# Kernel tuning notes

Measured on AMD Instinct MI355X. Metric: run time of the kernel, lower is better.

Reference implementation:

```python
import jax, jax.numpy as jnp
import numpy as np

N, E, D, H = 50000, 800000, 128, 4
C = D // H  # per-head out channels
NEG_SLOPE = 0.2
BN_EPS = 1e-5


def _glorot(key, shape, fan):
    return jax.random.normal(key, shape, jnp.float32) / np.sqrt(fan)


def setup_inputs() -> dict:
    key = jax.random.key(0)
    ks = jax.random.split(key, 8)
    inp = {
        'x': jax.random.normal(ks[0], (N, D), jnp.float32),
        'edge_index': jax.random.randint(ks[1], (2, E), 0, N, dtype=jnp.int32),
        'Wl1': _glorot(ks[2], (D, D), D), 'Wr1': _glorot(ks[3], (D, D), D),
        'att1': _glorot(ks[4], (H, C), C), 'b1': jnp.zeros((D,), jnp.float32),
        'gamma1': jnp.ones((D,), jnp.float32), 'beta1': jnp.zeros((D,), jnp.float32),
        'Wl2': _glorot(ks[5], (D, D), D), 'Wr2': _glorot(ks[6], (D, D), D),
        'att2': _glorot(ks[7], (H, C), C), 'b2': jnp.zeros((D,), jnp.float32),
        'gamma2': jnp.ones((D,), jnp.float32), 'beta2': jnp.zeros((D,), jnp.float32),
    }
    return inp


def gatv2_conv(x, src, dst, Wl, Wr, att, bias):
    # PyG GATv2Conv, concat=True, add_self_loops handled by caller.
    n = x.shape[0]
    xl = (x @ Wl).reshape(n, H, C)  # source-side transform
    xr = (x @ Wr).reshape(n, H, C)  # target-side transform
    e = xl[src] + xr[dst]                      # [E', H, C]
    e = jnp.where(e > 0, e, NEG_SLOPE * e)     # LeakyReLU
    logits = jnp.einsum('ehc,hc->eh', e, att)  # [E', H]
    # segment softmax over destination node
    m = jax.ops.segment_max(logits, dst, num_segments=n)  # [N, H]
    ex = jnp.exp(logits - m[dst])
    den = jax.ops.segment_sum(ex, dst, num_segments=n)
    alpha = ex / den[dst]                      # [E', H]
    out = jax.ops.segment_sum(alpha[:, :, None] * xl[src], dst, num_segments=n)
    return out.reshape(n, H * C) + bias


def batchnorm(x, gamma, beta):
    mu = x.mean(0)
    var = x.var(0)
    return gamma * (x - mu) * jax.lax.rsqrt(var + BN_EPS) + beta


def reference(x, edge_index, Wl1, Wr1, att1, b1, gamma1, beta1,
              Wl2, Wr2, att2, b2, gamma2, beta2):
    n = x.shape[0]
    loop = jnp.arange(n, dtype=edge_index.dtype)
    src = jnp.concatenate([edge_index[0], loop])  # add self-loops (PyG default)
    dst = jnp.concatenate([edge_index[1], loop])
    identity = x
    out = gatv2_conv(x, src, dst, Wl1, Wr1, att1, b1)
    out = jax.nn.relu(batchnorm(out, gamma1, beta1))
    out = gatv2_conv(out, src, dst, Wl2, Wr2, att2, b2)
    out = batchnorm(out, gamma2, beta2) + identity
    return jax.nn.relu(out)
```

## Files before the change

kernel.cpp:

```cpp
#include <hip/hip_runtime.h>
#include <cstdint>
#include <cstddef>

#define D 128
#define BN_EPS 1e-5f
#define NEG_INF -3.0e38f
#define BN_BLOCKS 512

typedef __attribute__((ext_vector_type(8))) short bf16x8;
typedef __attribute__((ext_vector_type(4))) float f32x4;

static __device__ __forceinline__ unsigned short f2bf(float f) {
    uint32_t u = __float_as_uint(f);
    uint32_t r = (u + 0x7fffu + ((u >> 16) & 1u)) >> 16;
    return (unsigned short)r;
}

static __device__ __forceinline__ float hsum16(float x) {
    x += __int_as_float(__builtin_amdgcn_update_dpp(0, __float_as_int(x), 0xB1, 0xF, 0xF, true));
    x += __int_as_float(__builtin_amdgcn_update_dpp(0, __float_as_int(x), 0x4E, 0xF, 0xF, true));
    x += __int_as_float(__builtin_amdgcn_update_dpp(0, __float_as_int(x), 0x124, 0xF, 0xF, true));
    x += __int_as_float(__builtin_amdgcn_update_dpp(0, __float_as_int(x), 0x128, 0xF, 0xF, true));
    return x;
}

__global__ void zero_kernel(int* cnt, int n, int* esrc_tail) {
    int i = blockIdx.x * 256 + threadIdx.x;
    if (i < n) cnt[i] = 0;
    if (i < 16) esrc_tail[i] = 0;
}

__global__ void hist_kernel(const int* __restrict__ dst, int* __restrict__ cnt, int E) {
    int e = blockIdx.x * 256 + threadIdx.x;
    if (e < E) atomicAdd(&cnt[dst[e]], 1);
}

__global__ void scan_block(const int* __restrict__ cnt, int* __restrict__ row_start,
                           int* __restrict__ bsum, int n) {
    __shared__ int tmp[256];
    int tid = threadIdx.x;
    int i = blockIdx.x * 256 + tid;
    int v = (i < n) ? cnt[i] : 0;
    tmp[tid] = v; __syncthreads();
    for (int off = 1; off < 256; off <<= 1) {
        int t = (tid >= off) ? tmp[tid - off] : 0;
        __syncthreads();
        tmp[tid] += t; __syncthreads();
    }
    if (i < n) row_start[i + 1] = tmp[tid];
    if (tid == 255) bsum[blockIdx.x] = tmp[255];
}

__global__ void scan_bsum(int* bsum, int nb) {
    __shared__ int tmp[256];
    int tid = threadIdx.x;
    int v = (tid < nb) ? bsum[tid] : 0;
    tmp[tid] = v; __syncthreads();
    for (int off = 1; off < 256; off <<= 1) {
        int t = (tid >= off) ? tmp[tid - off] : 0;
        __syncthreads();
        tmp[tid] += t; __syncthreads();
    }
    if (tid < nb) bsum[tid] = tmp[tid];
}

__global__ void scan_fix(int* __restrict__ row_start, const int* __restrict__ bsum,
                         int* __restrict__ cursor, int n) {
    int i = blockIdx.x * 256 + threadIdx.x;
    if (i < n) {
        int add = (blockIdx.x > 0) ? bsum[blockIdx.x - 1] : 0;
        int val = row_start[i + 1] + add;
        row_start[i + 1] = val;
        if (i + 1 < n) cursor[i + 1] = val;
    }
    if (i == 0) { row_start[0] = 0; cursor[0] = 0; }
}

__global__ void scatter_kernel(const int* __restrict__ src, const int* __restrict__ dst,
                               int* __restrict__ cursor, int* __restrict__ esrc, int E) {
    int e = blockIdx.x * 256 + threadIdx.x;
    if (e < E) {
        int p = atomicAdd(&cursor[dst[e]], 1);
        esrc[p] = src[e];
    }
}

__global__ void repack_w(const float* __restrict__ Wl, const float* __restrict__ Wr,
                         unsigned short* __restrict__ Bp) {
    int idx = blockIdx.x * 256 + threadIdx.x;
    int i    = idx & 7;
    int lane = (idx >> 3) & 63;
    int kt   = (idx >> 9) & 3;
    int jt   = idx >> 11;
    int k   = kt * 32 + (lane >> 4) * 8 + i;
    int col = jt * 16 + (lane & 15);
    float v = (col < 128) ? Wl[k * 128 + col] : Wr[k * 128 + (col - 128)];
    Bp[idx] = f2bf(v);
}

template<bool BN>
__global__ __launch_bounds__(256, 2) void gemm_mfma(
    const float* __restrict__ X, const unsigned short* __restrict__ Bp,
    const float* __restrict__ scale, const float* __restrict__ shift,
    unsigned short* __restrict__ xl, float* __restrict__ xr, int n)
{
    __shared__ unsigned short smem[32768];
    {
        const float4* s = (const float4*)Bp;
        float4* d = (float4*)smem;
        #pragma unroll
        for (int it = 0; it < 16; ++it)
            d[it * 256 + threadIdx.x] = s[it * 256 + threadIdx.x];
    }
    __syncthreads();

    int wid = threadIdx.x >> 6, lane = threadIdx.x & 63;
    int nw = (n + 31) >> 5;
    int wrow = blockIdx.x * 4 + wid;
    if (wrow >= nw) return;
    int r0 = wrow * 32;
    int m = lane & 15, hi = lane >> 4;

    f32x4 accA[16], accB[16];
    #pragma unroll
    for (int jt = 0; jt < 16; ++jt) {
        accA[jt] = (f32x4){0.f, 0.f, 0.f, 0.f};
        accB[jt] = (f32x4){0.f, 0.f, 0.f, 0.f};
    }

    int rA = r0 + m;      if (rA > n - 1) rA = n - 1;
    int rB = r0 + 16 + m; if (rB > n - 1) rB = n - 1;
    const float* xrowA = X + (size_t)rA * D;
    const float* xrowB = X + (size_t)rB * D;

    #pragma unroll
    for (int kt = 0; kt < 4; ++kt) {
        int kb = kt * 32 + hi * 8;
        float sca[8], shf[8];
        if (BN) {
            float4 s0 = *(const float4*)(scale + kb);
            float4 s1 = *(const float4*)(scale + kb + 4);
            float4 h0 = *(const float4*)(shift + kb);
            float4 h1 = *(const float4*)(shift + kb + 4);
            sca[0]=s0.x; sca[1]=s0.y; sca[2]=s0.z; sca[3]=s0.w;
            sca[4]=s1.x; sca[5]=s1.y; sca[6]=s1.z; sca[7]=s1.w;
            shf[0]=h0.x; shf[1]=h0.y; shf[2]=h0.z; shf[3]=h0.w;
            shf[4]=h1.x; shf[5]=h1.y; shf[6]=h1.z; shf[7]=h1.w;
        }
        float4 a0 = *(const float4*)(xrowA + kb);
        float4 a1 = *(const float4*)(xrowA + kb + 4);
        float4 b0 = *(const float4*)(xrowB + kb);
        float4 b1 = *(const float4*)(xrowB + kb + 4);
        float avA[8] = {a0.x, a0.y, a0.z, a0.w, a1.x, a1.y, a1.z, a1.w};
        float avB[8] = {b0.x, b0.y, b0.z, b0.w, b1.x, b1.y, b1.z, b1.w};
        bf16x8 afragA, afragB;
        #pragma unroll
        for (int i = 0; i < 8; ++i) {
            float va = avA[i], vb = avB[i];
            if (BN) {
                va = fmaxf(va * sca[i] + shf[i], 0.f);
                vb = fmaxf(vb * sca[i] + shf[i], 0.f);
            }
            afragA[i] = (short)f2bf(va);
            afragB[i] = (short)f2bf(vb);
        }
        #pragma unroll
        for (int jt = 0; jt < 16; ++jt) {
            bf16x8 bfrag = *(const bf16x8*)(smem + (size_t)((jt * 4 + kt) * 64 + lane) * 8);
            accA[jt] = __builtin_amdgcn_mfma_f32_16x16x32_bf16(afragA, bfrag, accA[jt], 0, 0, 0);
            accB[jt] = __builtin_amdgcn_mfma_f32_16x16x32_bf16(afragB, bfrag, accB[jt], 0, 0, 0);
        }
    }

    #pragma unroll
    for (int jt = 0; jt < 16; ++jt) {
        int col = jt * 16 + m;
        #pragma unroll
        for (int r = 0; r < 4; ++r) {
            int rowA = r0 + hi * 4 + r;
            int rowB = rowA + 16;
            if (rowA < n) {
                float v = accA[jt][r];
                if (jt < 8) xl[(size_t)rowA * D + col] = f2bf(v);
                else        xr[(size_t)rowA * D + (col - 128)] = v;
            }
            if (rowB < n) {
                float v = accB[jt][r];
                if (jt < 8) xl[(size_t)rowB * D + col] = f2bf(v);
                else        xr[(size_t)rowB * D + (col - 128)] = v;
            }
        }
    }
}

__global__ __launch_bounds__(256) void gat_kernel(
    const unsigned short* __restrict__ xl, const float* __restrict__ xr,
    const float* __restrict__ att, const float* __restrict__ bias,
    const int* __restrict__ row_start, const int* __restrict__ esrc,
    float* __restrict__ h, int n)
{
    const float L2E = 1.44269504089f;
    int wid = threadIdx.x >> 6;
    int lane = threadIdx.x & 63;
    int v = blockIdx.x * 4 + wid;
    if (v >= n) return;

    int c0 = lane * 2;
    const uint32_t* xl32 = (const uint32_t*)xl;
    int p = row_start[v], pe = row_start[v + 1];

    uint32_t idxc[8];
    #pragma unroll
    for (int j = 0; j < 8; ++j) idxc[j] = (uint32_t)esrc[p + j];

    float a0 = att[c0] * L2E, a1 = att[c0 + 1] * L2E;
    float xr0 = xr[(size_t)v * D + c0];
    float xr1 = xr[(size_t)v * D + c0 + 1];
    uint32_t ws = xl32[((uint32_t)v << 6) + (uint32_t)lane];

    uint32_t wc[8];
    #pragma unroll
    for (int j = 0; j < 8; ++j) wc[j] = xl32[(idxc[j] << 6) + (uint32_t)lane];

    float sx0 = __uint_as_float(ws << 16);
    float sx1 = __uint_as_float(ws & 0xffff0000u);
    float t0 = sx0 + xr0; t0 = fmaxf(t0, 0.2f * t0);
    float t1 = sx1 + xr1; t1 = fmaxf(t1, 0.2f * t1);
    float m = hsum16(fmaf(a0, t0, a1 * t1));
    float den = 1.f;
    float acc0 = sx0, acc1 = sx1, acc0b = 0.f, acc1b = 0.f;

    for (int i = p; i < pe; i += 8) {
        int rem = pe - i;
        uint32_t idxn[8];
        #pragma unroll
        for (int j = 0; j < 8; ++j) idxn[j] = (uint32_t)esrc[i + 8 + j];

        float lg[8], x0v[8], x1v[8];
        #pragma unroll
        for (int j = 0; j < 8; ++j) {
            float x0 = __uint_as_float(wc[j] << 16);
            float x1 = __uint_as_float(wc[j] & 0xffff0000u);
            x0v[j] = x0; x1v[j] = x1;
            float f0 = x0 + xr0; f0 = fmaxf(f0, 0.2f * f0);
            float f1 = x1 + xr1; f1 = fmaxf(f1, 0.2f * f1);
            lg[j] = hsum16(fmaf(a0, f0, a1 * f1));
        }

        uint32_t wn[8];
        #pragma unroll
        for (int j = 0; j < 8; ++j) wn[j] = xl32[(idxn[j] << 6) + (uint32_t)lane];

        #pragma unroll
        for (int j = 0; j < 8; ++j) if (j >= rem) lg[j] = NEG_INF;
        float mx = fmaxf(fmaxf(fmaxf(lg[0], lg[1]), fmaxf(lg[2], lg[3])),
                         fmaxf(fmaxf(lg[4], lg[5]), fmaxf(lg[6], lg[7])));
        if (__any(mx > m + 8.f)) {
            float nm = fmaxf(m, mx);
            float sc = exp2f(m - nm);
            den *= sc; acc0 *= sc; acc1 *= sc; acc0b *= sc; acc1b *= sc;
            m = nm;
        }
        float pex[8];
        #pragma unroll
        for (int j = 0; j < 8; ++j) pex[j] = exp2f(lg[j] - m);
        den += ((pex[0] + pex[1]) + (pex[2] + pex[3])) + ((pex[4] + pex[5]) + (pex[6] + pex[7]));
        #pragma unroll
        for (int j = 0; j < 8; j += 2) {
            acc0  = fmaf(pex[j],     x0v[j],     acc0);
            acc1  = fmaf(pex[j],     x1v[j],     acc1);
            acc0b = fmaf(pex[j + 1], x0v[j + 1], acc0b);
            acc1b = fmaf(pex[j + 1], x1v[j + 1], acc1b);
        }
        #pragma unroll
        for (int j = 0; j < 8; ++j) wc[j] = wn[j];
    }
    float inv = 1.0f / den;
    h[(size_t)v * D + c0]     = (acc0 + acc0b) * inv + bias[c0];
    h[(size_t)v * D + c0 + 1] = (acc1 + acc1b) * inv + bias[c0 + 1];
}

__global__ __launch_bounds__(256) void bn_stats(const float* __restrict__ h,
                                                float* __restrict__ psum, float* __restrict__ psum2, int n)
{
    int c4 = threadIdx.x & 31;
    int ty = threadIdx.x >> 5;
    float sx = 0.f, sy = 0.f, sz = 0.f, sw = 0.f;
    float qx = 0.f, qy = 0.f, qz = 0.f, qw = 0.f;
    for (int r = blockIdx.x * 8 + ty; r < n; r += gridDim.x * 8) {
        float4 v = *(const float4*)(h + (size_t)r * D + c4 * 4);
        sx += v.x; sy += v.y; sz += v.z; sw += v.w;
        qx = fmaf(v.x, v.x, qx); qy = fmaf(v.y, v.y, qy);
        qz = fmaf(v.z, v.z, qz); qw = fmaf(v.w, v.w, qw);
    }
    __shared__ float4 smA[256], smB[256];
    smA[threadIdx.x] = make_float4(sx, sy, sz, sw);
    smB[threadIdx.x] = make_float4(qx, qy, qz, qw);
    __syncthreads();
    #pragma unroll
    for (int off = 128; off >= 32; off >>= 1) {
        if (threadIdx.x < off) {
            float4 a = smA[threadIdx.x], b = smA[threadIdx.x + off];
            smA[threadIdx.x] = make_float4(a.x + b.x, a.y + b.y, a.z + b.z, a.w + b.w);
            float4 c = smB[threadIdx.x], d2 = smB[threadIdx.x + off];
            smB[threadIdx.x] = make_float4(c.x + d2.x, c.y + d2.y, c.z + d2.z, c.w + d2.w);
        }
        __syncthreads();
    }
    if (threadIdx.x < 32) {
        ((float4*)psum)[blockIdx.x * 32 + threadIdx.x]  = smA[threadIdx.x];
        ((float4*)psum2)[blockIdx.x * 32 + threadIdx.x] = smB[threadIdx.x];
    }
}

__global__ __launch_bounds__(256) void bn_mid(const float* __restrict__ psum, const float* __restrict__ psum2,
                                              float* __restrict__ pmid, float* __restrict__ pmid2)
{
    int c4 = threadIdx.x & 31;
    int rg = threadIdx.x >> 5;
    float4 s = make_float4(0.f, 0.f, 0.f, 0.f), q = make_float4(0.f, 0.f, 0.f, 0.f);
    #pragma unroll
    for (int k = 0; k < 4; ++k) {
        int r = blockIdx.x * 32 + rg + k * 8;
        float4 a = ((const float4*)psum)[r * 32 + c4];
        float4 b = ((const float4*)psum2)[r * 32 + c4];
        s.x += a.x; s.y += a.y; s.z += a.z; s.w += a.w;
        q.x += b.x; q.y += b.y; q.z += b.z; q.w += b.w;
    }
    __shared__ float4 smA[256], smB[256];
    smA[threadIdx.x] = s; smB[threadIdx.x] = q;
    __syncthreads();
    #pragma unroll
    for (int off = 128; off >= 32; off >>= 1) {
        if (threadIdx.x < off) {
            float4 a = smA[threadIdx.x], b = smA[threadIdx.x + off];
            smA[threadIdx.x] = make_float4(a.x + b.x, a.y + b.y, a.z + b.z, a.w + b.w);
            float4 c = smB[threadIdx.x], d2 = smB[threadIdx.x + off];
            smB[threadIdx.x] = make_float4(c.x + d2.x, c.y + d2.y, c.z + d2.z, c.w + d2.w);
        }
        __syncthreads();
    }
    if (threadIdx.x < 32) {
        ((float4*)pmid)[blockIdx.x * 32 + threadIdx.x]  = smA[threadIdx.x];
        ((float4*)pmid2)[blockIdx.x * 32 + threadIdx.x] = smB[threadIdx.x];
    }
}

__global__ void bn_final(const float* __restrict__ psum, const float* __restrict__ psum2,
                         const float* __restrict__ gamma, const float* __restrict__ beta,
                         float* __restrict__ scale, float* __restrict__ shift,
                         float inv_n, int nblk)
{
    int c = threadIdx.x & 127;
    int half = threadIdx.x >> 7;
    float s = 0.f, s2 = 0.f;
    for (int b = half; b < nblk; b += 2) {
        s  += psum[b * 128 + c];
        s2 += psum2[b * 128 + c];
    }
    __shared__ float sm[256], sm2[256];
    sm[threadIdx.x] = s; sm2[threadIdx.x] = s2; __syncthreads();
    if (half == 0) {
        s  += sm[threadIdx.x + 128];
        s2 += sm2[threadIdx.x + 128];
        float mu = s * inv_n;
        float var = s2 * inv_n - mu * mu;
        float inv = rsqrtf(var + BN_EPS);
        float sc = gamma[c] * inv;
        scale[c] = sc;
        shift[c] = beta[c] - mu * sc;
    }
}

__global__ __launch_bounds__(256) void final_kernel(
    const float* __restrict__ h2, const float* __restrict__ x,
    const float* __restrict__ scale, const float* __restrict__ shift,
    float* __restrict__ out, int total)
{
    int i = blockIdx.x * 256 + threadIdx.x;
    if (i * 4 >= total) return;
    float4 hv = ((const float4*)h2)[i];
    float4 xv = ((const float4*)x)[i];
    int c = (i * 4) & 127;
    float4 o;
    o.x = fmaxf(hv.x * scale[c + 0] + shift[c + 0] + xv.x, 0.f);
    o.y = fmaxf(hv.y * scale[c + 1] + shift[c + 1] + xv.y, 0.f);
    o.z = fmaxf(hv.z * scale[c + 2] + shift[c + 2] + xv.z, 0.f);
    o.w = fmaxf(hv.w * scale[c + 3] + shift[c + 3] + xv.w, 0.f);
    ((float4*)out)[i] = o;
}

extern "C" void kernel_launch(void* const* d_in, const int* in_sizes, int n_in,
                              void* d_out, int out_size, void* d_ws, size_t ws_size,
                              hipStream_t stream)
{
    const float* x    = (const float*)d_in[0];
    const int*   ei   = (const int*)  d_in[1];
    const float* Wl1  = (const float*)d_in[2];
    const float* Wr1  = (const float*)d_in[3];
    const float* att1 = (const float*)d_in[4];
    const float* b1   = (const float*)d_in[5];
    const float* g1   = (const float*)d_in[6];
    const float* be1  = (const float*)d_in[7];
    const float* Wl2  = (const float*)d_in[8];
    const float* Wr2  = (const float*)d_in[9];
    const float* att2 = (const float*)d_in[10];
    const float* b2   = (const float*)d_in[11];
    const float* g2   = (const float*)d_in[12];
    const float* be2  = (const float*)d_in[13];
    float* out = (float*)d_out;

    int n = in_sizes[0] / D;
    int E = in_sizes[1] / 2;
    const int* e_src = ei;
    const int* e_dst = ei + E;

    char* w = (char*)d_ws;
    auto alloc = [&](size_t bytes) -> char* {
        char* p = w;
        w += (bytes + 255) / 256 * 256;
        return p;
    };
    unsigned short* xl = (unsigned short*)alloc((size_t)n * D * 2);
    float* xr          = (float*)alloc((size_t)n * D * 4);
    float* h           = (float*)alloc((size_t)n * D * 4);
    int* row_start     = (int*)alloc((size_t)(n + 1) * 4);
    int* cnt           = (int*)alloc((size_t)n * 4);
    int* cursor        = (int*)alloc((size_t)n * 4);
    int* esrc          = (int*)alloc((size_t)(E + 16) * 4);
    int* bsum          = (int*)alloc(256 * 4);
    float* bn          = (float*)alloc(4 * 128 * 4);
    float* psum        = (float*)alloc((size_t)BN_BLOCKS * 128 * 4);
    float* psum2       = (float*)alloc((size_t)BN_BLOCKS * 128 * 4);
    float* pmid        = (float*)alloc(16 * 128 * 4);
    float* pmid2       = (float*)alloc(16 * 128 * 4);
    unsigned short* Bp1 = (unsigned short*)alloc(32768 * 2);
    unsigned short* Bp2 = (unsigned short*)alloc(32768 * 2);

    int nb = (n + 255) / 256;
    int gemm_blocks = (((n + 31) / 32) + 3) / 4;

    zero_kernel<<<(n + 255) / 256, 256, 0, stream>>>(cnt, n, esrc + E);
    hist_kernel<<<(E + 255) / 256, 256, 0, stream>>>(e_dst, cnt, E);
    scan_block<<<nb, 256, 0, stream>>>(cnt, row_start, bsum, n);
    scan_bsum<<<1, 256, 0, stream>>>(bsum, nb);
    scan_fix<<<nb, 256, 0, stream>>>(row_start, bsum, cursor, n);
    scatter_kernel<<<(E + 255) / 256, 256, 0, stream>>>(e_src, e_dst, cursor, esrc, E);
    repack_w<<<128, 256, 0, stream>>>(Wl1, Wr1, Bp1);
    repack_w<<<128, 256, 0, stream>>>(Wl2, Wr2, Bp2);

    gemm_mfma<false><<<gemm_blocks, 256, 0, stream>>>(x, Bp1, nullptr, nullptr, xl, xr, n);
    gat_kernel<<<(n + 3) / 4, 256, 0, stream>>>(xl, xr, att1, b1, row_start, esrc, h, n);
    bn_stats<<<BN_BLOCKS, 256, 0, stream>>>(h, psum, psum2, n);
    bn_mid<<<16, 256, 0, stream>>>(psum, psum2, pmid, pmid2);
    bn_final<<<1, 256, 0, stream>>>(pmid, pmid2, g1, be1, bn + 0, bn + 128, 1.0f / n, 16);

    gemm_mfma<true><<<gemm_blocks, 256, 0, stream>>>(h, Bp2, bn + 0, bn + 128, xl, xr, n);
    gat_kernel<<<(n + 3) / 4, 256, 0, stream>>>(xl, xr, att2, b2, row_start, esrc, h, n);
    bn_stats<<<BN_BLOCKS, 256, 0, stream>>>(h, psum, psum2, n);
    bn_mid<<<16, 256, 0, stream>>>(psum, psum2, pmid, pmid2);
    bn_final<<<1, 256, 0, stream>>>(pmid, pmid2, g2, be2, bn + 256, bn + 384, 1.0f / n, 16);

    final_kernel<<<((n * D / 4) + 255) / 256, 256, 0, stream>>>(h, x, bn + 256, bn + 384, out, n * D);
}
```

Baseline: 279.9 us.

## Split GAT wave into four edge groups with 16-byte gathers and merged softmax

Restructures the per-node attention kernel so each 64-lane wave splits into four 16-lane groups. Each group handles a different neighbor and loads a full 256-byte bf16 row with uint4 loads, instead of every lane loading 4 bytes of one neighbor at a time. Each group keeps its own online-softmax state, and the four states are merged at the end with cross-lane shuffles and rescaling. This cuts the per-edge head reduction to two DPP steps and widens the memory transactions, but drops the explicit software prefetch of the next batch of neighbors and wastes lanes on low-degree nodes.

```diff
diff --git a/kernel.cpp b/kernel.cpp
--- a/kernel.cpp
+++ b/kernel.cpp
@@ -16,11 +16,9 @@
     return (unsigned short)r;
 }
 
-static __device__ __forceinline__ float hsum16(float x) {
+static __device__ __forceinline__ float qsum4(float x) {
     x += __int_as_float(__builtin_amdgcn_update_dpp(0, __float_as_int(x), 0xB1, 0xF, 0xF, true));
     x += __int_as_float(__builtin_amdgcn_update_dpp(0, __float_as_int(x), 0x4E, 0xF, 0xF, true));
-    x += __int_as_float(__builtin_amdgcn_update_dpp(0, __float_as_int(x), 0x124, 0xF, 0xF, true));
-    x += __int_as_float(__builtin_amdgcn_update_dpp(0, __float_as_int(x), 0x128, 0xF, 0xF, true));
     return x;
 }
 
@@ -204,80 +202,98 @@
     int lane = threadIdx.x & 63;
     int v = blockIdx.x * 4 + wid;
     if (v >= n) return;
-
-    int c0 = lane * 2;
-    const uint32_t* xl32 = (const uint32_t*)xl;
-    int p = row_start[v], pe = row_start[v + 1];
-
-    uint32_t idxc[8];
-    #pragma unroll
-    for (int j = 0; j < 8; ++j) idxc[j] = (uint32_t)esrc[p + j];
-
-    float a0 = att[c0] * L2E, a1 = att[c0 + 1] * L2E;
-    float xr0 = xr[(size_t)v * D + c0];
-    float xr1 = xr[(size_t)v * D + c0 + 1];
-    uint32_t ws = xl32[((uint32_t)v << 6) + (uint32_t)lane];
-
-    uint32_t wc[8];
-    #pragma unroll
-    for (int j = 0; j < 8; ++j) wc[j] = xl32[(idxc[j] << 6) + (uint32_t)lane];
-
-    float sx0 = __uint_as_float(ws << 16);
-    float sx1 = __uint_as_float(ws & 0xffff0000u);
-    float t0 = sx0 + xr0; t0 = fmaxf(t0, 0.2f * t0);
-    float t1 = sx1 + xr1; t1 = fmaxf(t1, 0.2f * t1);
-    float m = hsum16(fmaf(a0, t0, a1 * t1));
-    float den = 1.f;
-    float acc0 = sx0, acc1 = sx1, acc0b = 0.f, acc1b = 0.f;
-
-    for (int i = p; i < pe; i += 8) {
-        int rem = pe - i;
-        uint32_t idxn[8];
-        #pragma unroll
-        for (int j = 0; j < 8; ++j) idxn[j] = (uint32_t)esrc[i + 8 + j];
-
-        float lg[8], x0v[8], x1v[8];
-        #pragma unroll
-        for (int j = 0; j < 8; ++j) {
-            float x0 = __uint_as_float(wc[j] << 16);
-            float x1 = __uint_as_float(wc[j] & 0xffff0000u);
-            x0v[j] = x0; x1v[j] = x1;
-            float f0 = x0 + xr0; f0 = fmaxf(f0, 0.2f * f0);
-            float f1 = x1 + xr1; f1 = fmaxf(f1, 0.2f * f1);
-            lg[j] = hsum16(fmaf(a0, f0, a1 * f1));
-        }
-
-        uint32_t wn[8];
-        #pragma unroll
-        for (int j = 0; j < 8; ++j) wn[j] = xl32[(idxn[j] << 6) + (uint32_t)lane];
-
-        #pragma unroll
-        for (int j = 0; j < 8; ++j) if (j >= rem) lg[j] = NEG_INF;
-        float mx = fmaxf(fmaxf(fmaxf(lg[0], lg[1]), fmaxf(lg[2], lg[3])),
-                         fmaxf(fmaxf(lg[4], lg[5]), fmaxf(lg[6], lg[7])));
-        if (__any(mx > m + 8.f)) {
-            float nm = fmaxf(m, mx);
+    int g  = lane >> 4;
+    int il = lane & 15;
+
+    float xrv[8], av[8];
+    {
+        float4 xa = *(const float4*)(xr + (size_t)v * D + il * 8);
+        float4 xb = *(const float4*)(xr + (size_t)v * D + il * 8 + 4);
+        xrv[0]=xa.x; xrv[1]=xa.y; xrv[2]=xa.z; xrv[3]=xa.w;
+        xrv[4]=xb.x; xrv[5]=xb.y; xrv[6]=xb.z; xrv[7]=xb.w;
+        float4 aa = *(const float4*)(att + il * 8);
+        float4 ab = *(const float4*)(att + il * 8 + 4);
+        av[0]=aa.x*L2E; av[1]=aa.y*L2E; av[2]=aa.z*L2E; av[3]=aa.w*L2E;
+        av[4]=ab.x*L2E; av[5]=ab.y*L2E; av[6]=ab.z*L2E; av[7]=ab.w*L2E;
+    }
+
+    int p = row_start[v];
+    int deg = row_start[v + 1] - p;
+    int vcnt = deg + 1;
+
+    float m = NEG_INF, den = 0.f;
+    float acc[8] = {0.f, 0.f, 0.f, 0.f, 0.f, 0.f, 0.f, 0.f};
+
+    auto process = [&](uint4 q, bool valid) {
+        float x[8];
+        x[0] = __uint_as_float(q.x << 16); x[1] = __uint_as_float(q.x & 0xffff0000u);
+        x[2] = __uint_as_float(q.y << 16); x[3] = __uint_as_float(q.y & 0xffff0000u);
+        x[4] = __uint_as_float(q.z << 16); x[5] = __uint_as_float(q.z & 0xffff0000u);
+        x[6] = __uint_as_float(q.w << 16); x[7] = __uint_as_float(q.w & 0xffff0000u);
+        float d = 0.f;
+        #pragma unroll
+        for (int k = 0; k < 8; ++k) {
+            float f = x[k] + xrv[k];
+            f = fmaxf(f, 0.2f * f);
+            d = fmaf(av[k], f, d);
+        }
+        d = qsum4(d);
+        float lg = valid ? d : NEG_INF;
+        if (__any(lg > m + 8.f)) {
+            float nm = fmaxf(m, lg);
             float sc = exp2f(m - nm);
-            den *= sc; acc0 *= sc; acc1 *= sc; acc0b *= sc; acc1b *= sc;
+            den *= sc;
+            #pragma unroll
+            for (int k = 0; k < 8; ++k) acc[k] *= sc;
             m = nm;
         }
-        float pex[8];
-        #pragma unroll
-        for (int j = 0; j < 8; ++j) pex[j] = exp2f(lg[j] - m);
-        den += ((pex[0] + pex[1]) + (pex[2] + pex[3])) + ((pex[4] + pex[5]) + (pex[6] + pex[7]));
-        #pragma unroll
-        for (int j = 0; j < 8; j += 2) {
-            acc0  = fmaf(pex[j],     x0v[j],     acc0);
-            acc1  = fmaf(pex[j],     x1v[j],     acc1);
-            acc0b = fmaf(pex[j + 1], x0v[j + 1], acc0b);
-            acc1b = fmaf(pex[j + 1], x1v[j + 1], acc1b);
-        }
-        #pragma unroll
-        for (int j = 0; j < 8; ++j) wc[j] = wn[j];
-    }
-    float inv = 1.0f / den;
-    h[(size_t)v * D + c0]     = (acc0 + acc0b) * inv + bias[c0];
-    h[(size_t)v * D + c0 + 1] = (acc1 + acc1b) * inv + bias[c0 + 1];
+        float pex = valid ? exp2f(lg - m) : 0.f;
+        den += pex;
+        #pragma unroll
+        for (int k = 0; k < 8; ++k) acc[k] = fmaf(pex, x[k], acc[k]);
+    };
+
+    {
+        uint32_t u0 = (g == 0) ? (uint32_t)v : (uint32_t)esrc[p + g - 1];
+        bool val0 = g < vcnt;
+        uint4 q0 = *(const uint4*)(xl + ((size_t)u0 << 7) + il * 8);
+        process(q0, val0);
+    }
+    for (int base = 4; base < vcnt; base += 8) {
+        int iA = base + g, iB = base + 4 + g;
+        bool vA = iA < vcnt, vB = iB < vcnt;
+        uint32_t uA = vA ? (uint32_t)esrc[p + iA - 1] : 0u;
+        uint32_t uB = vB ? (uint32_t)esrc[p + iB - 1] : 0u;
+        uint4 qA = *(const uint4*)(xl + ((size_t)uA << 7) + il * 8);
+        uint4 qB = *(const uint4*)(xl + ((size_t)uB << 7) + il * 8);
+        process(qA, vA);
+        process(qB, vB);
+    }
+
+    float m2 = fmaxf(m, __shfl_xor(m, 16));
+    float M  = fmaxf(m2, __shfl_xor(m2, 32));
+    float sc = exp2f(m - M);
+    den *= sc;
+    den += __shfl_xor(den, 16);
+    den += __shfl_xor(den, 32);
+    #pragma unroll
+    for (int k = 0; k < 8; ++k) {
+        acc[k] *= sc;
+        acc[k] += __shfl_xor(acc[k], 16);
+        acc[k] += __shfl_xor(acc[k], 32);
+    }
+    if (g == 0) {
+        float inv = 1.f / den;
+        float4 ba = *(const float4*)(bias + il * 8);
+        float4 bb = *(const float4*)(bias + il * 8 + 4);
+        float4 o0, o1;
+        o0.x = fmaf(acc[0], inv, ba.x); o0.y = fmaf(acc[1], inv, ba.y);
+        o0.z = fmaf(acc[2], inv, ba.z); o0.w = fmaf(acc[3], inv, ba.w);
+        o1.x = fmaf(acc[4], inv, bb.x); o1.y = fmaf(acc[5], inv, bb.y);
+        o1.z = fmaf(acc[6], inv, bb.z); o1.w = fmaf(acc[7], inv, bb.w);
+        *(float4*)(h + (size_t)v * D + il * 8)     = o0;
+        *(float4*)(h + (size_t)v * D + il * 8 + 4) = o1;
+    }
 }
 
 __global__ __launch_bounds__(256) void bn_stats(const float* __restrict__ h,
```

New measurement: 265.0 us. 5.3% less time.
